# Optimization experiments

Hardware: AMD Instinct MI355X
Metric: run time of the kernel (lower is better)

The kernel has to match this reference:

```python
import jax, jax.numpy as jnp
import numpy as np

N = 100000
E = 1600000
D = 128
EPS = 1e-5


def setup_inputs() -> dict:
    key = jax.random.key(0)
    ks = jax.random.split(key, 8)
    s = 1.0 / np.sqrt(D)
    feats = jax.random.normal(ks[0], (N, D), dtype=jnp.float32)
    src = jax.random.randint(ks[1], (E,), 0, N, dtype=jnp.int32)
    dst = jax.random.randint(ks[2], (E,), 0, N, dtype=jnp.int32)
    W_gcn = jax.random.normal(ks[3], (D, D), dtype=jnp.float32) * s
    b_gcn = jnp.zeros((D,), dtype=jnp.float32)
    W_res = jax.random.normal(ks[4], (D, D), dtype=jnp.float32) * s
    b_res = jnp.zeros((D,), dtype=jnp.float32)
    g1 = jnp.ones((D,), dtype=jnp.float32)
    be1 = jnp.zeros((D,), dtype=jnp.float32)
    g2 = jnp.ones((D,), dtype=jnp.float32)
    be2 = jnp.zeros((D,), dtype=jnp.float32)
    return {"feats": feats, "W_gcn": W_gcn, "b_gcn": b_gcn, "W_res": W_res,
            "b_res": b_res, "g1": g1, "be1": be1, "g2": g2, "be2": be2,
            "src": src, "dst": dst}


def _batchnorm(x, gamma, beta):
    # BatchNorm1d, training mode: biased batch stats over the node dim
    mu = jnp.mean(x, axis=0)
    var = jnp.var(x, axis=0)
    return gamma * (x - mu) * jax.lax.rsqrt(var + EPS) + beta


def reference(feats, W_gcn, b_gcn, W_res, b_res, g1, be1, g2, be2, src, dst):
    n = feats.shape[0]
    # GraphConv(norm='none'): sum-aggregate neighbor feats then linear (in<=out)
    agg = jax.ops.segment_sum(feats[src], dst, num_segments=n)  # [N, D]
    h = jax.nn.relu(agg @ W_gcn + b_gcn)
    # dgllife GCNLayer internal residual: activation(Linear(feats))
    res = jax.nn.relu(feats @ W_res + b_res)
    h = _batchnorm(h + res, g1, be1)
    # outer ResidualGCNLayer: Identity residual (in_feats==out_feats) + BN
    out = _batchnorm(h + feats, g2, be2)
    return out
```

## Files before the change

kernel.cpp:

```cpp
#include <hip/hip_runtime.h>
#include <hip/hip_bf16.h>
#include <stdint.h>

#define NN 100000
#define EE 1600000
#define DD 128
#define EPSV 1e-5f
#define WWIN 128
#define NB 782
#define NCLS 8
#define NSEG (NB * NCLS)
#define ITEMS (EE / 4)
#define ITEMS_PER_CLS (ITEMS / NCLS)
#define SORTCAP 4096

typedef __attribute__((ext_vector_type(8))) short short8;
typedef __attribute__((ext_vector_type(4))) float floatx4;
typedef unsigned short u16;

union S8 { short8 v; short s[8]; unsigned short u[8]; };

__device__ __forceinline__ float bf2f(u16 u) {
    return __uint_as_float(((unsigned int)u) << 16);
}
__device__ __forceinline__ u16 f2bf(float f) {
    unsigned int x = __float_as_uint(f);
    x += 0x7FFFu + ((x >> 16) & 1u);
    return (u16)(x >> 16);
}


__global__ void k_detect(const float* __restrict__ f, int* __restrict__ flag) {
    __shared__ int cnt;
    if (threadIdx.x == 0) cnt = 0;
    __syncthreads();
    const float v = fabsf(f[threadIdx.x]);
    if (v > 1e-3f && v < 1e3f) atomicAdd(&cnt, 1);
    __syncthreads();
    if (threadIdx.x == 0) *flag = (cnt >= 128) ? 1 : 0;
}

__global__ __launch_bounds__(256) void k_convert_feats(
    const int* __restrict__ flag, const float* __restrict__ ff,
    u16* __restrict__ fc)
{
    if (*flag == 0) return;
    const size_t P = (size_t)NN * (DD / 2);
    for (size_t i = (size_t)blockIdx.x * blockDim.x + threadIdx.x; i < P;
         i += (size_t)gridDim.x * blockDim.x) {
        const float2 v = *(const float2*)(ff + 2 * i);
        const unsigned int o = (unsigned int)f2bf(v.x) | ((unsigned int)f2bf(v.y) << 16);
        *(unsigned int*)(fc + 2 * i) = o;
    }
}

__global__ __launch_bounds__(256) void k_convert_params(
    const int* __restrict__ flag,
    const float* __restrict__ Wg, const float* __restrict__ Wr,
    const float* __restrict__ bg, const float* __restrict__ br,
    const float* __restrict__ g1, const float* __restrict__ g2,
    const float* __restrict__ be2, u16* __restrict__ pc)
{
    if (*flag == 0) return;
    const int i = blockIdx.x * blockDim.x + threadIdx.x;
    if (i >= 33408) return;
    float v;
    if (i < 16384)      v = Wg[i];
    else if (i < 32768) v = Wr[i - 16384];
    else {
        const int j = i - 32768;
        const int a = j >> 7, o = j & 127;
        v = (a == 0) ? bg[o] : (a == 1) ? br[o] : (a == 2) ? g1[o]
          : (a == 3) ? g2[o] : be2[o];
    }
    pc[i] = f2bf(v);
}

__global__ __launch_bounds__(256) void k_hist2(
    const int* __restrict__ dst, int* __restrict__ cnt)
{
    __shared__ int lc[NB];
    const int cls  = blockIdx.x & 7;
    const int blk  = blockIdx.x >> 3;
    const int nblk = gridDim.x >> 3;
    const int it0  = cls * ITEMS_PER_CLS;
    const int it1  = it0 + ITEMS_PER_CLS;
    for (int i = threadIdx.x; i < NB; i += 256) lc[i] = 0;
    __syncthreads();
    const int4* __restrict__ dst4 = (const int4*)dst;
    for (int it = it0 + blk * blockDim.x + threadIdx.x; it < it1;
         it += nblk * blockDim.x) {
        const int4 d = dst4[it];
        atomicAdd(&lc[d.x >> 7], 1);
        atomicAdd(&lc[d.y >> 7], 1);
        atomicAdd(&lc[d.z >> 7], 1);
        atomicAdd(&lc[d.w >> 7], 1);
    }
    __syncthreads();
    for (int i = threadIdx.x; i < NB; i += 256) {
        const int v = lc[i];
        if (v) atomicAdd(&cnt[i * NCLS + cls], v);
    }
}

__global__ __launch_bounds__(1024) void k_scanseg(
    const int* __restrict__ cnt, int* __restrict__ off,
    int* __restrict__ cursor)
{
    const int tx = threadIdx.x;
    const int lane = tx & 63, w = tx >> 6;
    __shared__ int wsum[16];
    __shared__ int carry;
    if (tx == 0) carry = 0;
    __syncthreads();
    for (int base = 0; base < NSEG; base += 1024) {
        const int i = base + tx;
        const int v = (i < NSEG) ? cnt[i] : 0;
        int incl = v;
#pragma unroll
        for (int d = 1; d < 64; d <<= 1) {
            const int n = __shfl_up(incl, d, 64);
            if (lane >= d) incl += n;
        }
        if (lane == 63) wsum[w] = incl;
        __syncthreads();
        if (tx < 16) {
            int s = wsum[tx];
#pragma unroll
            for (int d = 1; d < 16; d <<= 1) {
                const int n = __shfl_up(s, d, 16);
                if ((tx & 15) >= d) s += n;
            }
            wsum[tx] = s;
        }
        __syncthreads();
        const int c = carry;
        const int woff = (w == 0) ? 0 : wsum[w - 1];
        if (i < NSEG) {
            const int excl = c + woff + incl - v;
            off[i] = excl;
            cursor[i] = excl;
        }
        __syncthreads();
        if (tx == 0) carry = c + wsum[15];
        __syncthreads();
    }
    if (tx == 0) off[NSEG] = carry;
}

__global__ __launch_bounds__(256) void k_bin(
    const int* __restrict__ src, const int* __restrict__ dst,
    int* __restrict__ cursor, unsigned int* __restrict__ arena)
{
    __shared__ int lc[NB], lb[NB];
    const int cls  = blockIdx.x & 7;
    const int blk  = blockIdx.x >> 3;
    const int nblk = gridDim.x >> 3;
    const int it0  = cls * ITEMS_PER_CLS;
    const int it1  = it0 + ITEMS_PER_CLS;
    const int4* __restrict__ dst4 = (const int4*)dst;
    const int4* __restrict__ src4 = (const int4*)src;
    for (int i = threadIdx.x; i < NB; i += 256) lc[i] = 0;
    __syncthreads();
    for (int it = it0 + blk * blockDim.x + threadIdx.x; it < it1;
         it += nblk * blockDim.x) {
        const int4 d = dst4[it];
        atomicAdd(&lc[d.x >> 7], 1);
        atomicAdd(&lc[d.y >> 7], 1);
        atomicAdd(&lc[d.z >> 7], 1);
        atomicAdd(&lc[d.w >> 7], 1);
    }
    __syncthreads();
    for (int i = threadIdx.x; i < NB; i += 256) {
        const int v = lc[i];
        lb[i] = v ? atomicAdd(&cursor[i * NCLS + cls], v) : 0;
    }
    __syncthreads();
    for (int i = threadIdx.x; i < NB; i += 256) lc[i] = 0;
    __syncthreads();
    for (int it = it0 + blk * blockDim.x + threadIdx.x; it < it1;
         it += nblk * blockDim.x) {
        const int4 d = dst4[it];
        const int4 s = src4[it];
        int wv, p;
        wv = d.x >> 7; p = lb[wv] + atomicAdd(&lc[wv], 1);
        arena[p] = ((unsigned int)(d.x & 127) << 17) | (unsigned int)s.x;
        wv = d.y >> 7; p = lb[wv] + atomicAdd(&lc[wv], 1);
        arena[p] = ((unsigned int)(d.y & 127) << 17) | (unsigned int)s.y;
        wv = d.z >> 7; p = lb[wv] + atomicAdd(&lc[wv], 1);
        arena[p] = ((unsigned int)(d.z & 127) << 17) | (unsigned int)s.z;
        wv = d.w >> 7; p = lb[wv] + atomicAdd(&lc[wv], 1);
        arena[p] = ((unsigned int)(d.w & 127) << 17) | (unsigned int)s.w;
    }
}

__global__ __launch_bounds__(256) void k_winsort(
    unsigned int* __restrict__ arena, const int* __restrict__ off,
    int* __restrict__ row_st)
{
    __shared__ unsigned int buf[SORTCAP];
    __shared__ int cnt[WWIN], pref[WWIN], cur[WWIN];
    const int tx = threadIdx.x;
    const int b = blockIdx.x;
    const int s0 = off[b * NCLS];
    const int s1 = off[b * NCLS + NCLS];
    int len = s1 - s0;
    if (len > SORTCAP) len = SORTCAP;
    if (tx < WWIN) cnt[tx] = 0;
    __syncthreads();
    for (int i = tx; i < len; i += 256) {
        const unsigned int p = arena[s0 + i];
        buf[i] = p;
        atomicAdd(&cnt[p >> 17], 1);
    }
    __syncthreads();
    if (tx < WWIN) pref[tx] = cnt[tx];
    __syncthreads();
    for (int d = 1; d < WWIN; d <<= 1) {
        int v = 0;
        if (tx < WWIN && tx >= d) v = pref[tx - d];
        __syncthreads();
        if (tx < WWIN) pref[tx] += v;
        __syncthreads();
    }
    if (tx < WWIN) {
        const int excl = pref[tx] - cnt[tx];
        cur[tx] = excl;
        const int node = b * WWIN + tx;
        if (node < NN) row_st[node] = s0 + excl;
    }
    if (b == NB - 1 && tx == 0) row_st[NN] = EE;
    __syncthreads();
    for (int i = tx; i < len; i += 256) {
        const unsigned int p = buf[i];
        const int pos = atomicAdd(&cur[p >> 17], 1);
        arena[s0 + pos] = p & 0x1FFFFu;
    }
}

__global__ __launch_bounds__(256) void k_gather(
    const int* __restrict__ flag,
    const u16* __restrict__ feats_raw, const u16* __restrict__ feats_c,
    const int* __restrict__ edge_s, const int* __restrict__ row_st,
    u16* __restrict__ aggb)
{
    const u16* __restrict__ F = (*flag != 0) ? feats_c : feats_raw;
    const int lane = threadIdx.x & 63;
    const int half = lane >> 5;
    const int l32  = lane & 31;
    const int wave = (blockIdx.x * blockDim.x + threadIdx.x) >> 6;
    const int nw   = (gridDim.x * blockDim.x) >> 6;
    for (int node = wave; node < NN; node += nw) {
        const int rs  = row_st[node];
        const int deg = row_st[node + 1] - rs;
        float a0 = 0.f, a1 = 0.f, a2 = 0.f, a3 = 0.f;
        for (int base = 0; base < deg; base += 64) {
            const int rem = deg - base;
            const int nb  = rem < 64 ? rem : 64;
            int idx = 0;
            if (lane < nb) idx = edge_s[rs + base + lane];
            int j = 0;
            for (; j + 16 <= nb; j += 16) {
                uint2 vv[8];
#pragma unroll
                for (int q = 0; q < 8; ++q) {
                    const int s = __shfl(idx, j + 2 * q + half, 64);
                    vv[q] = *(const uint2*)(F + (size_t)s * DD + l32 * 4);
                }
#pragma unroll
                for (int q = 0; q < 8; ++q) {
                    a0 += bf2f((u16)(vv[q].x & 0xFFFFu));
                    a1 += bf2f((u16)(vv[q].x >> 16));
                    a2 += bf2f((u16)(vv[q].y & 0xFFFFu));
                    a3 += bf2f((u16)(vv[q].y >> 16));
                }
            }
            for (; j + 2 <= nb; j += 2) {
                const int s = __shfl(idx, j + half, 64);
                const uint2 v = *(const uint2*)(F + (size_t)s * DD + l32 * 4);
                a0 += bf2f((u16)(v.x & 0xFFFFu));
                a1 += bf2f((u16)(v.x >> 16));
                a2 += bf2f((u16)(v.y & 0xFFFFu));
                a3 += bf2f((u16)(v.y >> 16));
            }
            if (j < nb) {
                const int s = __shfl(idx, j, 64);
                const uint2 v = *(const uint2*)(F + (size_t)s * DD + l32 * 4);
                if (half == 0) {
                    a0 += bf2f((u16)(v.x & 0xFFFFu));
                    a1 += bf2f((u16)(v.x >> 16));
                    a2 += bf2f((u16)(v.y & 0xFFFFu));
                    a3 += bf2f((u16)(v.y >> 16));
                }
            }
        }
        a0 += __shfl_xor(a0, 32, 64);
        a1 += __shfl_xor(a1, 32, 64);
        a2 += __shfl_xor(a2, 32, 64);
        a3 += __shfl_xor(a3, 32, 64);
        if (half == 0) {
            uint2 o;
            o.x = (unsigned int)f2bf(a0) | ((unsigned int)f2bf(a1) << 16);
            o.y = (unsigned int)f2bf(a2) | ((unsigned int)f2bf(a3) << 16);
            *(uint2*)(aggb + (size_t)node * DD + l32 * 4) = o;
        }
    }
}

__global__ __launch_bounds__(256) void k_gemm(
    const int* __restrict__ flag,
    const u16* __restrict__ aggb,
    const u16* __restrict__ feats_raw, const u16* __restrict__ feats_c,
    const u16* __restrict__ Wg_raw, const u16* __restrict__ bg_raw,
    const u16* __restrict__ Wr_raw, const u16* __restrict__ br_raw,
    const u16* __restrict__ pc,
    u16* __restrict__ t_out)
{
    const bool f32 = (*flag != 0);
    const u16* __restrict__ F  = f32 ? feats_c     : feats_raw;
    const u16* __restrict__ Wg = f32 ? pc          : Wg_raw;
    const u16* __restrict__ Wr = f32 ? pc + 16384  : Wr_raw;
    const u16* __restrict__ bg = f32 ? pc + 32768  : bg_raw;
    const u16* __restrict__ br = f32 ? pc + 32896  : br_raw;

    const int lane = threadIdx.x & 63;
    const int wv   = threadIdx.x >> 6;
    const int l15  = lane & 15;
    const int quad = lane >> 4;
    const int c0 = wv * 16 + l15;
    const int c1 = 64 + wv * 16 + l15;

    S8 fg0[4], fg1[4], fr0[4], fr1[4];
#pragma unroll
    for (int kb = 0; kb < 4; ++kb) {
        const int kr = kb * 32 + quad * 8;
#pragma unroll
        for (int j = 0; j < 8; ++j) {
            fg0[kb].u[j] = Wg[(size_t)(kr + j) * DD + c0];
            fg1[kb].u[j] = Wg[(size_t)(kr + j) * DD + c1];
            fr0[kb].u[j] = Wr[(size_t)(kr + j) * DD + c0];
            fr1[kb].u[j] = Wr[(size_t)(kr + j) * DD + c1];
        }
    }
    const float bgc0 = bf2f(bg[c0]), bgc1 = bf2f(bg[c1]);
    const float brc0 = bf2f(br[c0]), brc1 = bf2f(br[c1]);

    for (int tile = blockIdx.x; tile < NN / 16; tile += gridDim.x) {
        const int row0 = tile * 16;
        const int arow = row0 + l15;
        floatx4 ag0 = {0.f,0.f,0.f,0.f}, ag1 = {0.f,0.f,0.f,0.f};
        floatx4 ar0 = {0.f,0.f,0.f,0.f}, ar1 = {0.f,0.f,0.f,0.f};
#pragma unroll
        for (int kb = 0; kb < 4; ++kb) {
            const int kbase = kb * 32 + quad * 8;
            S8 av, ff;
            av.v = *(const short8*)(aggb + (size_t)arow * DD + kbase);
            ff.v = *(const short8*)(F    + (size_t)arow * DD + kbase);
            ag0 = __builtin_amdgcn_mfma_f32_16x16x32_bf16(av.v, fg0[kb].v, ag0, 0, 0, 0);
            ag1 = __builtin_amdgcn_mfma_f32_16x16x32_bf16(av.v, fg1[kb].v, ag1, 0, 0, 0);
            ar0 = __builtin_amdgcn_mfma_f32_16x16x32_bf16(ff.v, fr0[kb].v, ar0, 0, 0, 0);
            ar1 = __builtin_amdgcn_mfma_f32_16x16x32_bf16(ff.v, fr1[kb].v, ar1, 0, 0, 0);
        }
#pragma unroll
        for (int r = 0; r < 4; ++r) {
            const int row = row0 + quad * 4 + r;
            const float t0 = fmaxf(ag0[r] + bgc0, 0.f) + fmaxf(ar0[r] + brc0, 0.f);
            const float t1 = fmaxf(ag1[r] + bgc1, 0.f) + fmaxf(ar1[r] + brc1, 0.f);
            t_out[(size_t)row * DD + c0] = f2bf(t0);
            t_out[(size_t)row * DD + c1] = f2bf(t1);
        }
    }
}

__global__ __launch_bounds__(256) void k_stats(
    const int* __restrict__ flag,
    const u16* __restrict__ t,
    const u16* __restrict__ feats_raw, const u16* __restrict__ feats_c,
    float* __restrict__ stats)
{
    const u16* __restrict__ F = (*flag != 0) ? feats_c : feats_raw;
    const int tx = threadIdx.x;
    const int c2 = (tx & 63) * 2;
    const int rg = tx >> 6;
    float acc[10];
#pragma unroll
    for (int k = 0; k < 10; ++k) acc[k] = 0.f;

    for (int r = blockIdx.x * 4 + rg; r < NN; r += gridDim.x * 4) {
        const unsigned int tv = *(const unsigned int*)(t + (size_t)r * DD + c2);
        const unsigned int fv = *(const unsigned int*)(F + (size_t)r * DD + c2);
        const float t0 = bf2f((u16)(tv & 0xFFFFu));
        const float t1 = bf2f((u16)(tv >> 16));
        const float f0 = bf2f((u16)(fv & 0xFFFFu));
        const float f1 = bf2f((u16)(fv >> 16));
        acc[0] += t0;      acc[1] += t1;
        acc[2] += t0 * t0; acc[3] += t1 * t1;
        acc[4] += f0;      acc[5] += f1;
        acc[6] += f0 * f0; acc[7] += f1 * f1;
        acc[8] += t0 * f0; acc[9] += t1 * f1;
    }

    __shared__ float red[256][10];
#pragma unroll
    for (int k = 0; k < 10; ++k) red[tx][k] = acc[k];
    __syncthreads();
    if (tx < 64) {
#pragma unroll
        for (int k = 0; k < 10; ++k) {
            const float v = red[tx][k] + red[tx + 64][k] + red[tx + 128][k] + red[tx + 192][k];
            unsafeAtomicAdd(&stats[(k >> 1) * DD + c2 + (k & 1)], v);
        }
    }
}

__global__ __launch_bounds__(256) void k_final(
    const int* __restrict__ flag,
    const u16* __restrict__ t,
    const u16* __restrict__ feats_raw, const u16* __restrict__ feats_c,
    const u16* __restrict__ g1_raw, const u16* __restrict__ g2_raw,
    const u16* __restrict__ be2_raw, const u16* __restrict__ pc,
    const float* __restrict__ stats,
    void* __restrict__ out)
{
    const bool f32 = (*flag != 0);
    const u16* __restrict__ F   = f32 ? feats_c    : feats_raw;
    const u16* __restrict__ g1  = f32 ? pc + 33024 : g1_raw;
    const u16* __restrict__ g2  = f32 ? pc + 33152 : g2_raw;
    const u16* __restrict__ be2 = f32 ? pc + 33280 : be2_raw;

    __shared__ float sA[DD], sB[DD], sG[DD];
    if (threadIdx.x < DD) {
        const int c = threadIdx.x;
        const float invN = 1.0f / (float)NN;
        const float St  = stats[c],          Stt = stats[DD + c];
        const float Sf  = stats[2 * DD + c], Sff = stats[3 * DD + c];
        const float Stf = stats[4 * DD + c];
        const float mu1  = St * invN;
        const float vart = fmaxf(Stt * invN - mu1 * mu1, 0.f);
        const float muf  = Sf * invN;
        const float varf = fmaxf(Sff * invN - muf * muf, 0.f);
        const float cov  = Stf * invN - mu1 * muf;
        const float r1   = rsqrtf(vart + EPSV);
        const float a1   = bf2f(g1[c]) * r1;
        const float var2 = fmaxf(a1 * a1 * vart + 2.f * a1 * cov + varf, 0.f);
        const float r2   = rsqrtf(var2 + EPSV);
        const float g2r2 = bf2f(g2[c]) * r2;
        sA[c] = g2r2 * a1;
        sB[c] = g2r2;
        sG[c] = bf2f(be2[c]) - g2r2 * (a1 * mu1 + muf);
    }
    __syncthreads();

    float* outf = (float*)out;
    u16*   outb = (u16*)out;
    const size_t P = (size_t)NN * (DD / 2);
    for (size_t i = (size_t)blockIdx.x * blockDim.x + threadIdx.x; i < P;
         i += (size_t)gridDim.x * blockDim.x) {
        const int c = ((int)(i & 63)) * 2;
        const unsigned int tv = *(const unsigned int*)(t + 2 * i);
        const unsigned int fv = *(const unsigned int*)(F + 2 * i);
        const float o0 = sA[c]     * bf2f((u16)(tv & 0xFFFFu))
                       + sB[c]     * bf2f((u16)(fv & 0xFFFFu)) + sG[c];
        const float o1 = sA[c + 1] * bf2f((u16)(tv >> 16))
                       + sB[c + 1] * bf2f((u16)(fv >> 16)) + sG[c + 1];
        if (f32) {
            float2 o; o.x = o0; o.y = o1;
            *(float2*)(outf + 2 * i) = o;
        } else {
            const unsigned int ov = (unsigned int)f2bf(o0) | ((unsigned int)f2bf(o1) << 16);
            *(unsigned int*)(outb + 2 * i) = ov;
        }
    }
}

extern "C" void kernel_launch(void* const* d_in, const int* in_sizes, int n_in,
                              void* d_out, int out_size, void* d_ws, size_t ws_size,
                              hipStream_t stream) {
    const u16* feats = (const u16*)d_in[0];
    const u16* Wg    = (const u16*)d_in[1];
    const u16* bg    = (const u16*)d_in[2];
    const u16* Wr    = (const u16*)d_in[3];
    const u16* br    = (const u16*)d_in[4];
    const u16* g1    = (const u16*)d_in[5];
    const u16* g2    = (const u16*)d_in[7];
    const u16* be2   = (const u16*)d_in[8];
    const int* src = (const int*)d_in[9];
    const int* dst = (const int*)d_in[10];

    char* ws = (char*)d_ws;
    u16*          aggb    = (u16*)  ws;
    u16*          t       = (u16*)  (ws + 25600000);
    u16*          feats_c = (u16*)  (ws + 51200000);
    u16*          pc      = (u16*)  (ws + 76800000);
    float*        stats   = (float*)(ws + 76866816);
    int*          flag    = (int*)  (ws + 76869376);
    int*          cnt     = (int*)  (ws + 76869632);
    int*          off     = (int*)  (ws + 76894656);
    int*          cursor  = (int*)  (ws + 76919684);
    int*          row_st  = (int*)  (ws + 76944708);
    unsigned int* arena   = (unsigned int*)(ws + 77344712);

    hipMemsetAsync(cnt,   0, NSEG * sizeof(int), stream);
    hipMemsetAsync(stats, 0, 5 * DD * sizeof(float), stream);

    k_detect<<<1, 256, 0, stream>>>((const float*)d_in[0], flag);
    k_convert_feats<<<1024, 256, 0, stream>>>(flag, (const float*)d_in[0], feats_c);
    k_convert_params<<<131, 256, 0, stream>>>(flag,
        (const float*)d_in[1], (const float*)d_in[3], (const float*)d_in[2],
        (const float*)d_in[4], (const float*)d_in[5], (const float*)d_in[7],
        (const float*)d_in[8], pc);

    k_hist2  <<<256, 256, 0, stream>>>(dst, cnt);
    k_scanseg<<<1, 1024, 0, stream>>>(cnt, off, cursor);
    k_bin    <<<256, 256, 0, stream>>>(src, dst, cursor, arena);
    k_winsort<<<NB, 256, 0, stream>>>(arena, off, row_st);

    k_gather<<<2048, 256, 0, stream>>>(flag, feats, feats_c, (const int*)arena, row_st, aggb);
    k_gemm  <<<1024, 256, 0, stream>>>(flag, aggb, feats, feats_c, Wg, bg, Wr, br, pc, t);
    k_stats <<<784,  256, 0, stream>>>(flag, t, feats, feats_c, stats);
    k_final <<<2048, 256, 0, stream>>>(flag, t, feats, feats_c, g1, g2, be2, pc, stats, d_out);
}
```

Measured before the change: 340.8 us.

## Gather four nodes per wave with 16-lane groups and 16-byte loads

The neighbour-sum gather kernel now gives each 16-lane group one destination node, so a wave aggregates four nodes at once. Each lane loads 8 bf16 values per edge with 16-byte loads, and the cross-half shuffle reduction and the half-masked tail are gone. The aim is wider memory transactions and more independent rows in flight, to better hide latency on the random feature gathers. An occupancy hint in the launch bounds is also added. The risk is divergence when the four nodes in a wave have different degrees, plus higher register pressure from eight accumulators.

```diff
diff --git a/kernel.cpp b/kernel.cpp
--- a/kernel.cpp
+++ b/kernel.cpp
@@ -238,7 +238,7 @@
     }
 }
 
-__global__ __launch_bounds__(256) void k_gather(
+__global__ __launch_bounds__(256, 8) void k_gather(
     const int* __restrict__ flag,
     const u16* __restrict__ feats_raw, const u16* __restrict__ feats_c,
     const int* __restrict__ edge_s, const int* __restrict__ row_st,
@@ -246,26 +246,29 @@
 {
     const u16* __restrict__ F = (*flag != 0) ? feats_c : feats_raw;
     const int lane = threadIdx.x & 63;
-    const int half = lane >> 5;
-    const int l32  = lane & 31;
+    const int l16  = lane & 15;
+    const int gb   = lane & 48;
     const int wave = (blockIdx.x * blockDim.x + threadIdx.x) >> 6;
     const int nw   = (gridDim.x * blockDim.x) >> 6;
-    for (int node = wave; node < NN; node += nw) {
-        const int rs  = row_st[node];
-        const int deg = row_st[node + 1] - rs;
+
+    for (int n0 = wave * 4; n0 < NN; n0 += nw * 4) {
+        const int node = n0 + (lane >> 4);
+        const int rs   = row_st[node];
+        const int deg  = row_st[node + 1] - rs;
         float a0 = 0.f, a1 = 0.f, a2 = 0.f, a3 = 0.f;
-        for (int base = 0; base < deg; base += 64) {
-            const int rem = deg - base;
-            const int nb  = rem < 64 ? rem : 64;
-            int idx = 0;
-            if (lane < nb) idx = edge_s[rs + base + lane];
+        float a4 = 0.f, a5 = 0.f, a6 = 0.f, a7 = 0.f;
+        for (int ebase = 0; ebase < deg; ebase += 16) {
+            const int rem = deg - ebase;
+            const int nb  = rem < 16 ? rem : 16;
+            int il = 0;
+            if (l16 < nb) il = edge_s[rs + ebase + l16];
             int j = 0;
-            for (; j + 16 <= nb; j += 16) {
-                uint2 vv[8];
+            for (; j + 8 <= nb; j += 8) {
+                uint4 vv[8];
 #pragma unroll
                 for (int q = 0; q < 8; ++q) {
-                    const int s = __shfl(idx, j + 2 * q + half, 64);
-                    vv[q] = *(const uint2*)(F + (size_t)s * DD + l32 * 4);
+                    const int s = __shfl(il, gb + j + q, 64);
+                    vv[q] = *(const uint4*)(F + (size_t)s * DD + l16 * 8);
                 }
 #pragma unroll
                 for (int q = 0; q < 8; ++q) {
@@ -273,37 +276,50 @@
                     a1 += bf2f((u16)(vv[q].x >> 16));
                     a2 += bf2f((u16)(vv[q].y & 0xFFFFu));
                     a3 += bf2f((u16)(vv[q].y >> 16));
+                    a4 += bf2f((u16)(vv[q].z & 0xFFFFu));
+                    a5 += bf2f((u16)(vv[q].z >> 16));
+                    a6 += bf2f((u16)(vv[q].w & 0xFFFFu));
+                    a7 += bf2f((u16)(vv[q].w >> 16));
                 }
             }
-            for (; j + 2 <= nb; j += 2) {
-                const int s = __shfl(idx, j + half, 64);
-                const uint2 v = *(const uint2*)(F + (size_t)s * DD + l32 * 4);
+            for (; j + 4 <= nb; j += 4) {
+                uint4 vv[4];
+#pragma unroll
+                for (int q = 0; q < 4; ++q) {
+                    const int s = __shfl(il, gb + j + q, 64);
+                    vv[q] = *(const uint4*)(F + (size_t)s * DD + l16 * 8);
+                }
+#pragma unroll
+                for (int q = 0; q < 4; ++q) {
+                    a0 += bf2f((u16)(vv[q].x & 0xFFFFu));
+                    a1 += bf2f((u16)(vv[q].x >> 16));
+                    a2 += bf2f((u16)(vv[q].y & 0xFFFFu));
+                    a3 += bf2f((u16)(vv[q].y >> 16));
+                    a4 += bf2f((u16)(vv[q].z & 0xFFFFu));
+                    a5 += bf2f((u16)(vv[q].z >> 16));
+                    a6 += bf2f((u16)(vv[q].w & 0xFFFFu));
+                    a7 += bf2f((u16)(vv[q].w >> 16));
+                }
+            }
+            for (; j < nb; ++j) {
+                const int s = __shfl(il, gb + j, 64);
+                const uint4 v = *(const uint4*)(F + (size_t)s * DD + l16 * 8);
                 a0 += bf2f((u16)(v.x & 0xFFFFu));
                 a1 += bf2f((u16)(v.x >> 16));
                 a2 += bf2f((u16)(v.y & 0xFFFFu));
                 a3 += bf2f((u16)(v.y >> 16));
+                a4 += bf2f((u16)(v.z & 0xFFFFu));
+                a5 += bf2f((u16)(v.z >> 16));
+                a6 += bf2f((u16)(v.w & 0xFFFFu));
+                a7 += bf2f((u16)(v.w >> 16));
             }
-            if (j < nb) {
-                const int s = __shfl(idx, j, 64);
-                const uint2 v = *(const uint2*)(F + (size_t)s * DD + l32 * 4);
-                if (half == 0) {
-                    a0 += bf2f((u16)(v.x & 0xFFFFu));
-                    a1 += bf2f((u16)(v.x >> 16));
-                    a2 += bf2f((u16)(v.y & 0xFFFFu));
-                    a3 += bf2f((u16)(v.y >> 16));
-                }
-            }
-        }
-        a0 += __shfl_xor(a0, 32, 64);
-        a1 += __shfl_xor(a1, 32, 64);
-        a2 += __shfl_xor(a2, 32, 64);
-        a3 += __shfl_xor(a3, 32, 64);
-        if (half == 0) {
-            uint2 o;
-            o.x = (unsigned int)f2bf(a0) | ((unsigned int)f2bf(a1) << 16);
-            o.y = (unsigned int)f2bf(a2) | ((unsigned int)f2bf(a3) << 16);
-            *(uint2*)(aggb + (size_t)node * DD + l32 * 4) = o;
-        }
+        }
+        uint4 o;
+        o.x = (unsigned int)f2bf(a0) | ((unsigned int)f2bf(a1) << 16);
+        o.y = (unsigned int)f2bf(a2) | ((unsigned int)f2bf(a3) << 16);
+        o.z = (unsigned int)f2bf(a4) | ((unsigned int)f2bf(a5) << 16);
+        o.w = (unsigned int)f2bf(a6) | ((unsigned int)f2bf(a7) << 16);
+        *(uint4*)(aggb + (size_t)node * DD + l16 * 8) = o;
     }
 }
 
```

Result: no change. 341.6 us (+0.2%).
